# Kernel tuning notes

Measured on AMD Instinct MI355X. Metric: run time of the kernel, lower is better.

## Reference

```python
import jax, jax.numpy as jnp
import numpy as np

WS = (7, 7)      # window_size
SS = (3, 3)      # shift_size
NH = 6           # num_heads


def _rel_index(ws):
    # Faithful to define_relative_position_index (including its quirk of
    # summing raw signed offsets, which can be negative -> wraparound gather).
    coords = jnp.stack(jnp.meshgrid(jnp.arange(ws[0]), jnp.arange(ws[1]), indexing='ij'))  # (2,w0,w1)
    flat = coords.reshape(2, -1)                       # (2,N)
    rel = flat[:, :, None] - flat[:, None, :]          # (2,N,N)
    return rel.sum(axis=0).reshape(-1)                 # (N*N,)


def setup_inputs() -> dict:
    key = jax.random.key(0)
    ks = jax.random.split(key, 6)
    C, H, W = 192, 448, 448
    return {
        'x': jax.random.normal(ks[0], (C, H, W), dtype=jnp.float32),
        'qkv_weight': jax.random.normal(ks[1], (3 * C, C), dtype=jnp.float32) * 0.05,
        'qkv_bias': jax.random.normal(ks[2], (3 * C,), dtype=jnp.float32) * 0.02,
        'proj_weight': jax.random.normal(ks[3], (C, C), dtype=jnp.float32) * 0.05,
        'proj_bias': jax.random.normal(ks[4], (C,), dtype=jnp.float32) * 0.02,
        'rel_bias_table': jax.random.normal(ks[5], ((2 * WS[0] - 1) * (2 * WS[1] - 1), NH), dtype=jnp.float32) * 0.02,
    }


def reference(x, qkv_weight, qkv_bias, proj_weight, proj_bias, rel_bias_table):
    C, H, W = x.shape
    w0, w1 = WS
    s0, s1 = SS
    N = w0 * w1
    hd = C // NH
    nW = (H // w0) * (W // w1)

    # relative position bias: (NH, N, N)
    idx = _rel_index(WS)
    bias = rel_bias_table[idx].reshape(N, N, NH).transpose(2, 0, 1)

    xh = jnp.transpose(x, (1, 2, 0))                          # (H,W,C)
    xh = jnp.roll(xh, (-s0, -s1), axis=(0, 1))                # cyclic shift
    xw = xh.reshape(H // w0, w0, W // w1, w1, C)
    xw = xw.transpose(0, 2, 1, 3, 4).reshape(nW, N, C)        # window partition

    qkv = xw @ qkv_weight.T + qkv_bias                        # (nW,N,3C)
    qkv = qkv.reshape(nW, N, 3, NH, hd).transpose(2, 0, 3, 1, 4)
    q = qkv[0] * (hd ** -0.5)
    k = qkv[1]
    v = qkv[2]

    attn = jnp.einsum('whnd,whmd->whnm', q, k) + bias         # (nW,NH,N,N)

    # shift attention mask (region buckets 0..8, value row*3+col)
    rb = (jnp.arange(H) >= H - w0).astype(jnp.int32) + (jnp.arange(H) >= H - s0).astype(jnp.int32)
    cb = (jnp.arange(W) >= W - w1).astype(jnp.int32) + (jnp.arange(W) >= W - s1).astype(jnp.int32)
    img = rb[:, None] * 3 + cb[None, :]                       # (H,W)
    m = img.reshape(H // w0, w0, W // w1, w1).transpose(0, 2, 1, 3).reshape(nW, N)
    amask = jnp.where(m[:, None, :] - m[:, :, None] == 0, 0.0, -100.0)  # (nW,N,N)
    attn = attn + amask[:, None, :, :]

    attn = jax.nn.softmax(attn, axis=-1)                      # attention_dropout p=0 -> identity

    out = jnp.einsum('whnm,whmd->whnd', attn, v)              # (nW,NH,N,hd)
    out = out.transpose(0, 2, 1, 3).reshape(nW, N, C)
    out = out @ proj_weight.T + proj_bias                     # dropout p=0 -> identity

    out = out.reshape(H // w0, W // w1, w0, w1, C)
    out = out.transpose(0, 2, 1, 3, 4).reshape(H, W, C)       # reverse window partition
    out = jnp.roll(out, (s0, s1), axis=(0, 1))                # reverse cyclic shift
    return jnp.transpose(out, (2, 0, 1))                      # back to (C,H,W)
```

## Files before the change

### kernel.cpp

```cpp
#include <hip/hip_runtime.h>


typedef short s16x8 __attribute__((ext_vector_type(8)));
typedef float f32x4 __attribute__((ext_vector_type(4)));
typedef unsigned short u16x4 __attribute__((ext_vector_type(4)));

#define C_DIM 192
#define H_DIM 448
#define W_DIM 448
#define HW    (H_DIM * W_DIM)
#define NHEAD 6
#define NTOK  49
#define MT    64

#define XW_S 200
#define AO_S 200
#define QH_S 40
#define KH_S 40
#define VT_S 72
#define PH_S 72

__device__ __forceinline__ unsigned short f2bf(float f) {
  unsigned u = __float_as_uint(f);
  u = (u + 0x7fffu + ((u >> 16) & 1u)) >> 16;
  return (unsigned short)u;
}

__global__ void pack_wqkv(const float* __restrict__ w, unsigned short* __restrict__ dst) {
  int g = blockIdx.x * blockDim.x + threadIdx.x;
  if (g >= 13824) return;
  int lane = g & 63;
  int t1 = g >> 6;
  int kk = t1 % 6;  t1 /= 6;
  int dt = t1 & 1;  t1 >>= 1;
  int which = t1 % 3;
  int h = t1 / 3;
  int n  = which * 192 + h * 32 + dt * 16 + (lane & 15);
  int kb = kk * 32 + (lane >> 4) * 8;
  const float* src = w + n * 192 + kb;
  unsigned short* d = dst + g * 8;
#pragma unroll
  for (int j = 0; j < 8; j++) d[j] = f2bf(src[j]);
}

__global__ void pack_wproj(const float* __restrict__ w, unsigned short* __restrict__ dst) {
  int g = blockIdx.x * blockDim.x + threadIdx.x;
  if (g >= 4608) return;
  int lane = g & 63;
  int t1 = g >> 6;
  int kk = t1 % 6;
  int nt = t1 / 6;
  int n  = nt * 16 + (lane & 15);
  int kb = kk * 32 + (lane >> 4) * 8;
  const float* src = w + n * 192 + kb;
  unsigned short* d = dst + g * 8;
#pragma unroll
  for (int j = 0; j < 8; j++) d[j] = f2bf(src[j]);
}

__global__ void bias_prep(const float* __restrict__ table, float* __restrict__ dst) {
  int t = blockIdx.x * blockDim.x + threadIdx.x;
  if (t >= 6 * 64 * 64) return;
  int j = t & 63;
  int i = (t >> 6) & 63;
  int h = t >> 12;
  float v = 0.f;
  if (i < NTOK && j < NTOK) {
    int s = (i / 7 - j / 7) + (i % 7 - j % 7);
    if (s < 0) s += 169;
    v = table[s * 6 + h];
  }
  dst[t] = v;
}

__global__ __launch_bounds__(256, 2) void swin_fused(
    const float* __restrict__ x,
    const float* __restrict__ qkv_bias,
    const float* __restrict__ proj_bias,
    const unsigned short* __restrict__ wqkv_p,
    const unsigned short* __restrict__ wproj_p,
    const float* __restrict__ biasM,
    float* __restrict__ out) {
  __shared__ __align__(16) unsigned short xw[MT * XW_S];
  __shared__ __align__(16) unsigned short ao[MT * AO_S];
  __shared__ __align__(16) unsigned short qh[MT * QH_S];
  __shared__ __align__(16) unsigned short kh[MT * KH_S];
  __shared__ __align__(16) unsigned short vth[32 * VT_S];
  __shared__ __align__(16) unsigned short Ph[MT * PH_S];
  __shared__ int mreg[MT];

  const int tid  = threadIdx.x;
  const int lane = tid & 63;
  const int wid  = tid >> 6;
  const int l16  = lane & 15;
  const int quad = lane >> 4;
  const int wr   = blockIdx.x >> 6;
  const int wc   = blockIdx.x & 63;

  for (int task = tid; task < 1344; task += 256) {
    int c = task / 7;
    int i = task % 7;
    int r = wr * 7 + i + 3; if (r >= H_DIM) r -= H_DIM;
    const float* src = x + c * HW + r * W_DIM;
    int cb = wc * 7 + 3;
#pragma unroll
    for (int j = 0; j < 7; j++) {
      int w = cb + j; if (w >= W_DIM) w -= W_DIM;
      xw[(i * 7 + j) * XW_S + c] = f2bf(src[w]);
    }
  }
  for (int idx = tid; idx < 15 * C_DIM; idx += 256)
    xw[(NTOK + idx / C_DIM) * XW_S + (idx % C_DIM)] = 0;
  if (tid < MT) {
    int v = 99;
    if (tid < NTOK) {
      int gi = wr * 7 + tid / 7, gj = wc * 7 + tid % 7;
      int rb = (gi >= 441) + (gi >= 445);
      int cb = (gj >= 441) + (gj >= 445);
      v = rb * 3 + cb;
    }
    mreg[tid] = v;
  }
  __syncthreads();

  const float scale = 0.17677669529663687f;

  for (int h = 0; h < NHEAD; h++) {
    for (int e = wid; e < 6; e += 4) {
      int which = e >> 1;
      int dt = e & 1;
      s16x8 bf[6];
      const s16x8* wp = (const s16x8*)wqkv_p;
      int base = (((h * 3 + which) * 2 + dt) * 6) * 64 + lane;
#pragma unroll
      for (int kk = 0; kk < 6; kk++) bf[kk] = wp[base + kk * 64];
      int ncol = which * 192 + h * 32 + dt * 16 + l16;
      float bias = qkv_bias[ncol];
      int dl = dt * 16 + l16;
#pragma unroll
      for (int mt = 0; mt < 4; mt++) {
        f32x4 acc = {0.f, 0.f, 0.f, 0.f};
#pragma unroll
        for (int kk = 0; kk < 6; kk++) {
          s16x8 a = *(const s16x8*)&xw[(mt * 16 + l16) * XW_S + kk * 32 + quad * 8];
          acc = __builtin_amdgcn_mfma_f32_16x16x32_bf16(a, bf[kk], acc, 0, 0, 0);
        }
        int t0 = mt * 16 + quad * 4;
        if (which == 0) {
#pragma unroll
          for (int r = 0; r < 4; r++) qh[(t0 + r) * QH_S + dl] = f2bf(acc[r] + bias);
        } else if (which == 1) {
#pragma unroll
          for (int r = 0; r < 4; r++) kh[(t0 + r) * KH_S + dl] = f2bf(acc[r] + bias);
        } else {
          u16x4 pv;
#pragma unroll
          for (int r = 0; r < 4; r++) pv[r] = f2bf(acc[r] + bias);
          *(u16x4*)&vth[dl * VT_S + t0] = pv;
        }
      }
    }
    __syncthreads();

    {
      const int mt = wid;
      s16x8 aq = *(const s16x8*)&qh[(mt * 16 + l16) * QH_S + quad * 8];
      f32x4 sc[4];
#pragma unroll
      for (int nt = 0; nt < 4; nt++) {
        s16x8 bk = *(const s16x8*)&kh[(nt * 16 + l16) * KH_S + quad * 8];
        f32x4 z = {0.f, 0.f, 0.f, 0.f};
        sc[nt] = __builtin_amdgcn_mfma_f32_16x16x32_bf16(aq, bk, z, 0, 0, 0);
      }
      float sv[4][4];
#pragma unroll
      for (int nt = 0; nt < 4; nt++) {
        int j = nt * 16 + l16;
        int mj = mreg[j];
        float mpad = (j >= NTOK) ? -30000.f : 0.f;
#pragma unroll
        for (int r = 0; r < 4; r++) {
          int i = mt * 16 + quad * 4 + r;
          float s = sc[nt][r] * scale + biasM[(h * 64 + i) * 64 + j];
          s += (mreg[i] == mj) ? 0.f : -100.f;
          sv[r][nt] = s + mpad;
        }
      }
#pragma unroll
      for (int r = 0; r < 4; r++) {
        float mx = fmaxf(fmaxf(sv[r][0], sv[r][1]), fmaxf(sv[r][2], sv[r][3]));
#pragma unroll
        for (int off = 1; off < 16; off <<= 1) mx = fmaxf(mx, __shfl_xor(mx, off));
        float e0 = __expf(sv[r][0] - mx), e1 = __expf(sv[r][1] - mx);
        float e2 = __expf(sv[r][2] - mx), e3 = __expf(sv[r][3] - mx);
        float sm = e0 + e1 + e2 + e3;
#pragma unroll
        for (int off = 1; off < 16; off <<= 1) sm += __shfl_xor(sm, off);
        float inv = 1.f / sm;
        int i = mt * 16 + quad * 4 + r;
        Ph[i * PH_S +  0 + l16] = f2bf(e0 * inv);
        Ph[i * PH_S + 16 + l16] = f2bf(e1 * inv);
        Ph[i * PH_S + 32 + l16] = f2bf(e2 * inv);
        Ph[i * PH_S + 48 + l16] = f2bf(e3 * inv);
      }
    }

    {
      const int mt = wid;
      s16x8 ap0 = *(const s16x8*)&Ph[(mt * 16 + l16) * PH_S + quad * 8];
      s16x8 ap1 = *(const s16x8*)&Ph[(mt * 16 + l16) * PH_S + 32 + quad * 8];
#pragma unroll
      for (int dtv = 0; dtv < 2; dtv++) {
        s16x8 bv0 = *(const s16x8*)&vth[(dtv * 16 + l16) * VT_S + quad * 8];
        s16x8 bv1 = *(const s16x8*)&vth[(dtv * 16 + l16) * VT_S + 32 + quad * 8];
        f32x4 acc = {0.f, 0.f, 0.f, 0.f};
        acc = __builtin_amdgcn_mfma_f32_16x16x32_bf16(ap0, bv0, acc, 0, 0, 0);
        acc = __builtin_amdgcn_mfma_f32_16x16x32_bf16(ap1, bv1, acc, 0, 0, 0);
        int t0 = mt * 16 + quad * 4;
#pragma unroll
        for (int r = 0; r < 4; r++)
          ao[(t0 + r) * AO_S + h * 32 + dtv * 16 + l16] = f2bf(acc[r]);
      }
    }
    __syncthreads();
  }

  for (int nt = wid; nt < 12; nt += 4) {
    s16x8 bf[6];
    const s16x8* wp = (const s16x8*)wproj_p;
    int base = nt * 6 * 64 + lane;
#pragma unroll
    for (int kk = 0; kk < 6; kk++) bf[kk] = wp[base + kk * 64];
    int cout = nt * 16 + l16;
    float pb = proj_bias[cout];
#pragma unroll
    for (int mt = 0; mt < 4; mt++) {
      f32x4 acc = {0.f, 0.f, 0.f, 0.f};
#pragma unroll
      for (int kk = 0; kk < 6; kk++) {
        s16x8 a = *(const s16x8*)&ao[(mt * 16 + l16) * AO_S + kk * 32 + quad * 8];
        acc = __builtin_amdgcn_mfma_f32_16x16x32_bf16(a, bf[kk], acc, 0, 0, 0);
      }
      int t0 = mt * 16 + quad * 4;
#pragma unroll
      for (int r = 0; r < 4; r++) {
        int t = t0 + r;
        if (t < NTOK) {
          int i = t / 7, j = t % 7;
          int R = wr * 7 + i + 3;  if (R >= H_DIM) R -= H_DIM;
          int Cc = wc * 7 + j + 3; if (Cc >= W_DIM) Cc -= W_DIM;
          out[cout * HW + R * W_DIM + Cc] = acc[r] + pb;
        }
      }
    }
  }
}

extern "C" void kernel_launch(void* const* d_in, const int* in_sizes, int n_in,
                              void* d_out, int out_size, void* d_ws, size_t ws_size,
                              hipStream_t stream) {
  const float* x     = (const float*)d_in[0];
  const float* wqkv  = (const float*)d_in[1];
  const float* bqkv  = (const float*)d_in[2];
  const float* wproj = (const float*)d_in[3];
  const float* bproj = (const float*)d_in[4];
  const float* table = (const float*)d_in[5];

  unsigned short* wqkv_p = (unsigned short*)d_ws;
  unsigned short* wproj_p = wqkv_p + 110592;
  float* biasM = (float*)(wproj_p + 36864);

  pack_wqkv<<<54, 256, 0, stream>>>(wqkv, wqkv_p);
  pack_wproj<<<18, 256, 0, stream>>>(wproj, wproj_p);
  bias_prep<<<96, 256, 0, stream>>>(table, biasM);
  swin_fused<<<4096, 256, 0, stream>>>(x, bqkv, bproj, wqkv_p, wproj_p, biasM,
                                       (float*)d_out);
}
```

Before: 644.7 us.

## Pre-transpose input to channel-last bf16 and stage output through transposed buffer

Adds a separate kernel that applies the cyclic shift and transposes x into a channel-last bf16 buffer, so the fused kernel can load each window's tokens with contiguous 16-byte global-to-LDS loads instead of strided scalar reads. Depending on workspace size, the output is also written channel-last (fp32 or bf16) and a second transpose kernel scatters it back to CHW layout with coalesced stores. This trades the uncoalesced per-window gathers and scatters for extra full-tensor passes through memory and extra kernel launches. The bf16 output mode also adds a rounding step on the result.

```diff
diff --git a/kernel.cpp b/kernel.cpp
--- a/kernel.cpp
+++ b/kernel.cpp
@@ -24,6 +24,12 @@
   unsigned u = __float_as_uint(f);
   u = (u + 0x7fffu + ((u >> 16) & 1u)) >> 16;
   return (unsigned short)u;
+}
+
+__device__ __forceinline__ void gl_lds16(const void* g, void* l) {
+  __builtin_amdgcn_global_load_lds(
+      (const __attribute__((address_space(1))) void*)g,
+      (__attribute__((address_space(3))) void*)l, 16, 0, 0);
 }
 
 __global__ void pack_wqkv(const float* __restrict__ w, unsigned short* __restrict__ dst) {
@@ -73,13 +79,68 @@
   dst[t] = v;
 }
 
+__global__ __launch_bounds__(256) void transpose_in(
+    const float* __restrict__ x, unsigned short* __restrict__ xT) {
+  __shared__ __align__(16) unsigned short tile[64 * XW_S];
+  const int hw0 = blockIdx.x * 64;
+  const int col = threadIdx.x & 63;
+  const int hw = hw0 + col;
+#pragma unroll 8
+  for (int c = threadIdx.x >> 6; c < 192; c += 4)
+    tile[col * XW_S + c] = f2bf(x[c * HW + hw]);
+  __syncthreads();
+  const int r = hw0 / W_DIM;
+  const int wbase = hw0 % W_DIM;
+  int rp = r + (H_DIM - 3); if (rp >= H_DIM) rp -= H_DIM;
+  for (int t = threadIdx.x; t < 64 * 24; t += 256) {
+    int cc = t / 24, c8 = t % 24;
+    int w = wbase + cc;
+    int wp = w + (W_DIM - 3); if (wp >= W_DIM) wp -= W_DIM;
+    *(s16x8*)(xT + ((rp * W_DIM + wp) * 192 + c8 * 8)) =
+        *(const s16x8*)&tile[cc * XW_S + c8 * 8];
+  }
+}
+
+template <int MODE>
+__global__ __launch_bounds__(256) void transpose_out(
+    const void* __restrict__ oT, float* __restrict__ out) {
+  __shared__ __align__(16) float tile[64 * 196];
+  const int hw0 = blockIdx.x * 64;
+  if (MODE == 0) {
+    const float* p = (const float*)oT;
+    for (int t = threadIdx.x; t < 64 * 48; t += 256) {
+      int cc = t / 48, c4 = t % 48;
+      *(f32x4*)&tile[cc * 196 + c4 * 4] =
+          *(const f32x4*)(p + (hw0 + cc) * 192 + c4 * 4);
+    }
+  } else {
+    const unsigned short* p = (const unsigned short*)oT;
+    for (int t = threadIdx.x; t < 64 * 24; t += 256) {
+      int cc = t / 24, c8 = t % 24;
+      s16x8 v = *(const s16x8*)(p + (hw0 + cc) * 192 + c8 * 8);
+#pragma unroll
+      for (int k = 0; k < 8; k++)
+        tile[cc * 196 + c8 * 8 + k] =
+            __uint_as_float(((unsigned)(unsigned short)v[k]) << 16);
+    }
+  }
+  __syncthreads();
+  const int col = threadIdx.x & 63;
+#pragma unroll 8
+  for (int c = threadIdx.x >> 6; c < 192; c += 4)
+    out[c * HW + hw0 + col] = tile[col * 196 + c];
+}
+
+template <int MODE>
 __global__ __launch_bounds__(256, 2) void swin_fused(
     const float* __restrict__ x,
+    const unsigned short* __restrict__ xT,
     const float* __restrict__ qkv_bias,
     const float* __restrict__ proj_bias,
     const unsigned short* __restrict__ wqkv_p,
     const unsigned short* __restrict__ wproj_p,
     const float* __restrict__ biasM,
+    void* __restrict__ outT,
     float* __restrict__ out) {
   __shared__ __align__(16) unsigned short xw[MT * XW_S];
   __shared__ __align__(16) unsigned short ao[MT * AO_S];
@@ -97,20 +158,37 @@
   const int wr   = blockIdx.x >> 6;
   const int wc   = blockIdx.x & 63;
 
-  for (int task = tid; task < 1344; task += 256) {
-    int c = task / 7;
-    int i = task % 7;
-    int r = wr * 7 + i + 3; if (r >= H_DIM) r -= H_DIM;
-    const float* src = x + c * HW + r * W_DIM;
-    int cb = wc * 7 + 3;
-#pragma unroll
-    for (int j = 0; j < 7; j++) {
-      int w = cb + j; if (w >= W_DIM) w -= W_DIM;
-      xw[(i * 7 + j) * XW_S + c] = f2bf(src[w]);
-    }
-  }
-  for (int idx = tid; idx < 15 * C_DIM; idx += 256)
-    xw[(NTOK + idx / C_DIM) * XW_S + (idx % C_DIM)] = 0;
+  if (MODE != 3) {
+    const unsigned short* xTw = xT + ((wr * 7) * W_DIM + wc * 7) * 192;
+    for (int base = wid * 64; base < 1225; base += 256) {
+      int t = base + lane;
+      if (t < 1225) {
+        int tok = t / 25, c8 = t % 25;
+        int i = tok / 7, j = tok % 7;
+        const unsigned short* g =
+            (c8 == 24) ? xTw : xTw + (i * W_DIM + j) * 192 + c8 * 8;
+        gl_lds16(g, &xw[base * 8]);
+      }
+    }
+    s16x8 zz = {0, 0, 0, 0, 0, 0, 0, 0};
+    for (int idx = tid; idx < 375; idx += 256)
+      *(s16x8*)&xw[(1225 + idx) * 8] = zz;
+  } else {
+    for (int task = tid; task < 1344; task += 256) {
+      int c = task / 7;
+      int i = task % 7;
+      int r = wr * 7 + i + 3; if (r >= H_DIM) r -= H_DIM;
+      const float* src = x + c * HW + r * W_DIM;
+      int cb = wc * 7 + 3;
+#pragma unroll
+      for (int j = 0; j < 7; j++) {
+        int w = cb + j; if (w >= W_DIM) w -= W_DIM;
+        xw[(i * 7 + j) * XW_S + c] = f2bf(src[w]);
+      }
+    }
+    for (int idx = tid; idx < 15 * C_DIM; idx += 256)
+      xw[(NTOK + idx / C_DIM) * XW_S + (idx % C_DIM)] = 0;
+  }
   if (tid < MT) {
     int v = 99;
     if (tid < NTOK) {
@@ -249,7 +327,14 @@
           int i = t / 7, j = t % 7;
           int R = wr * 7 + i + 3;  if (R >= H_DIM) R -= H_DIM;
           int Cc = wc * 7 + j + 3; if (Cc >= W_DIM) Cc -= W_DIM;
-          out[cout * HW + R * W_DIM + Cc] = acc[r] + pb;
+          float v = acc[r] + pb;
+          if (MODE == 2 || MODE == 3) {
+            out[cout * HW + R * W_DIM + Cc] = v;
+          } else if (MODE == 0) {
+            ((float*)outT)[(R * W_DIM + Cc) * 192 + cout] = v;
+          } else {
+            ((unsigned short*)outT)[(R * W_DIM + Cc) * 192 + cout] = f2bf(v);
+          }
         }
       }
     }
@@ -265,14 +350,47 @@
   const float* wproj = (const float*)d_in[3];
   const float* bproj = (const float*)d_in[4];
   const float* table = (const float*)d_in[5];
+  float* out = (float*)d_out;
 
   unsigned short* wqkv_p = (unsigned short*)d_ws;
   unsigned short* wproj_p = wqkv_p + 110592;
   float* biasM = (float*)(wproj_p + 36864);
+  const size_t base_b = 393216;
+  const size_t xT_b = (size_t)HW * 192 * 2;
+  const size_t oT32_b = (size_t)HW * 192 * 4;
+  unsigned short* xT = (unsigned short*)((char*)d_ws + base_b);
+  void* outT = (char*)d_ws + base_b + xT_b;
+
+  int mode;
+  if (ws_size >= base_b + xT_b + oT32_b) mode = 0;
+  else if (ws_size >= base_b + xT_b + xT_b) mode = 1;
+  else if (ws_size >= base_b + xT_b) mode = 2;
+  else mode = 3;
 
   pack_wqkv<<<54, 256, 0, stream>>>(wqkv, wqkv_p);
   pack_wproj<<<18, 256, 0, stream>>>(wproj, wproj_p);
   bias_prep<<<96, 256, 0, stream>>>(table, biasM);
-  swin_fused<<<4096, 256, 0, stream>>>(x, bqkv, bproj, wqkv_p, wproj_p, biasM,
-                                       (float*)d_out);
-}
+  if (mode != 3)
+    transpose_in<<<HW / 64, 256, 0, stream>>>(x, xT);
+
+  switch (mode) {
+    case 0:
+      swin_fused<0><<<4096, 256, 0, stream>>>(x, xT, bqkv, bproj, wqkv_p,
+                                              wproj_p, biasM, outT, out);
+      transpose_out<0><<<HW / 64, 256, 0, stream>>>(outT, out);
+      break;
+    case 1:
+      swin_fused<1><<<4096, 256, 0, stream>>>(x, xT, bqkv, bproj, wqkv_p,
+                                              wproj_p, biasM, outT, out);
+      transpose_out<1><<<HW / 64, 256, 0, stream>>>(outT, out);
+      break;
+    case 2:
+      swin_fused<2><<<4096, 256, 0, stream>>>(x, xT, bqkv, bproj, wqkv_p,
+                                              wproj_p, biasM, outT, out);
+      break;
+    default:
+      swin_fused<3><<<4096, 256, 0, stream>>>(x, xT, bqkv, bproj, wqkv_p,
+                                              wproj_p, biasM, outT, out);
+      break;
+  }
+}
```

Result: faster. 583.6 us (-9.5%).
